# Kernel optimization log

Measured on AMD Instinct MI355X. Metric: run time of the kernel, lower is better.

## Reference

```python
import jax, jax.numpy as jnp
import numpy as np

GAMMA = 0.1
B, C, H, W = 8, 64, 64, 64
CINT = C // 8


def setup_inputs() -> dict:
    key = jax.random.key(0)
    ks = jax.random.split(key, 5)
    x = jax.random.normal(ks[0], (B, C, H, W), dtype=jnp.float32)
    Wq = jax.random.normal(ks[1], (CINT, C), dtype=jnp.float32) * 0.05
    Wk = jax.random.normal(ks[2], (CINT, C), dtype=jnp.float32) * 0.05
    Wv = jax.random.normal(ks[3], (CINT, C), dtype=jnp.float32) * 0.05
    Wout = jax.random.normal(ks[4], (C, CINT), dtype=jnp.float32) * 0.05
    return {"x": x, "Wq": Wq, "Wk": Wk, "Wv": Wv, "Wout": Wout}


def reference(x, Wq, Wk, Wv, Wout):
    b, c, h, w = x.shape
    n = h * w
    cint = Wq.shape[0]
    xf = x.reshape(b, c, n)                               # [B,C,N]
    q = jnp.einsum('ic,bcn->bin', Wq, xf)                 # [B,Cint,N]
    k = jnp.einsum('ic,bcn->bin', Wk, xf)
    v = jnp.einsum('ic,bcn->bin', Wv, xf)
    # scores[b, n, m] = q[b,:,n] . k[b,:,m]; softmax over dim=1 (the n axis)
    scores = jnp.einsum('bin,bim->bnm', q, k) / jnp.sqrt(jnp.asarray(cint, x.dtype))
    att = jax.nn.softmax(scores, axis=1)                  # [B,N,N], softmax over rows
    att_out = jnp.einsum('bin,bnm->bim', v, att)          # [B,Cint,N]
    out = jnp.einsum('ci,bim->bcm', Wout, att_out)        # [B,C,N]
    return x + out.reshape(b, c, h, w) * GAMMA
```

## Files before the change

### kernel.cpp

```cpp
#include <hip/hip_runtime.h>
#include <math.h>

#define BB 8
#define CC 64
#define NN 4096
#define CI 8
#define GAMMA 0.1f
#define SCALE (1.44269504088896f * 0.35355339059327f)
#define NSPLIT 8

typedef float v4f  __attribute__((ext_vector_type(4)));
typedef float v16f __attribute__((ext_vector_type(16)));
typedef __bf16 bf16x8 __attribute__((ext_vector_type(8)));
typedef unsigned int u32x2 __attribute__((ext_vector_type(2)));

__device__ __forceinline__ float fast_exp2(float x) {
    return __builtin_amdgcn_exp2f(x);
}

__device__ __forceinline__ unsigned int cvt_pk_bf16(float lo, float hi) {
    unsigned int r;
    asm("v_cvt_pk_bf16_f32 %0, %1, %2" : "=v"(r) : "v"(lo), "v"(hi));
    return r;
}

__global__ __launch_bounds__(256) void qkv_kernel(
        const float* __restrict__ x,
        const float* __restrict__ Wq, const float* __restrict__ Wk,
        const float* __restrict__ Wv,
        __bf16* __restrict__ qbh, __bf16* __restrict__ kbh,
        __bf16* __restrict__ vbh, float* __restrict__ attab) {
    __shared__ float sw[3 * CI * CC];
    __shared__ float xt[CC * 36];
    __shared__ unsigned short sq[32 * 8];
    __shared__ unsigned short sk[32 * 8];
    const int t = threadIdx.x;
    const int b  = blockIdx.y;
    const int n0 = blockIdx.x * 32;

    for (int idx = t; idx < CI * CC; idx += 256) {
        sw[idx]                = Wq[idx];
        sw[CI * CC + idx]      = Wk[idx] * SCALE;
        sw[2 * CI * CC + idx]  = Wv[idx];
    }
    {
        const float* xb = x + ((size_t)b * CC) * NN + n0;
#pragma unroll
        for (int j = 0; j < 2; ++j) {
            int u = t + j * 256;
            int c = u >> 3, n4 = u & 7;
            v4f xv = *(const v4f*)(xb + (size_t)c * NN + n4 * 4);
            *(v4f*)(xt + c * 36 + n4 * 4) = xv;
        }
    }
    int lin = (blockIdx.y * (NN / 32) + blockIdx.x) * 256 + t;
    for (int idx = lin; idx < BB * 9 * NN; idx += BB * NN * CI) attab[idx] = 0.f;
    __syncthreads();

    const int i  = t >> 5;
    const int nl = t & 31;
    const int n = n0 + nl;
    const v4f* wq4 = (const v4f*)(sw + i * CC);
    const v4f* wk4 = (const v4f*)(sw + CI * CC + i * CC);
    const v4f* wv4 = (const v4f*)(sw + 2 * CI * CC + i * CC);
    float qa = 0.f, ka = 0.f, va = 0.f;
#pragma unroll 4
    for (int c4 = 0; c4 < CC / 4; ++c4) {
        v4f wq = wq4[c4], wk = wk4[c4], wv = wv4[c4];
        float x0 = xt[(c4 * 4 + 0) * 36 + nl];
        float x1 = xt[(c4 * 4 + 1) * 36 + nl];
        float x2 = xt[(c4 * 4 + 2) * 36 + nl];
        float x3 = xt[(c4 * 4 + 3) * 36 + nl];
        qa = fmaf(wq.x, x0, qa); ka = fmaf(wk.x, x0, ka); va = fmaf(wv.x, x0, va);
        qa = fmaf(wq.y, x1, qa); ka = fmaf(wk.y, x1, ka); va = fmaf(wv.y, x1, va);
        qa = fmaf(wq.z, x2, qa); ka = fmaf(wk.z, x2, ka); va = fmaf(wv.z, x2, va);
        qa = fmaf(wq.w, x3, qa); ka = fmaf(wk.w, x3, ka); va = fmaf(wv.w, x3, va);
    }
    __bf16 vb = (__bf16)va;
    vbh[((size_t)b * CI + i) * NN + n] = vb;
    __bf16 qb = (__bf16)qa, kb2 = (__bf16)ka;
    sq[nl * 8 + i] = *(unsigned short*)&qb;
    sk[nl * 8 + i] = *(unsigned short*)&kb2;
    __syncthreads();
    if (t < 32) {
        *(uint4*)(qbh + ((size_t)b * NN + n0 + t) * 8) = *(const uint4*)(sq + t * 8);
        *(uint4*)(kbh + ((size_t)b * NN + n0 + t) * 8) = *(const uint4*)(sk + t * 8);
    }
}

__global__ __launch_bounds__(256) void att_kernel(
        const __bf16* __restrict__ qbh, const __bf16* __restrict__ kbh,
        const __bf16* __restrict__ vbh, float* __restrict__ attab) {
    const int t = threadIdx.x;
    const int w    = t >> 6;
    const int l    = t & 63;
    const int ln   = l & 31;
    const int hi   = l >> 5;
    const int b  = blockIdx.z;
    const int m0 = blockIdx.x * 128 + w * 32;
    const int nbase = blockIdx.y * (NN / NSPLIT);
    const int NCH = (NN / NSPLIT) / 32;

    bf16x8 zero8;
#pragma unroll
    for (int z = 0; z < 8; ++z) zero8[z] = (__bf16)0.0f;
    const v16f vzero = {0.f,0.f,0.f,0.f,0.f,0.f,0.f,0.f,
                        0.f,0.f,0.f,0.f,0.f,0.f,0.f,0.f};

    bf16x8 kfragB = hi ? zero8
                       : *(const bf16x8*)(kbh + ((size_t)b * NN + m0 + ln) * 8);

    const __bf16* qrow = qbh + (size_t)b * NN * 8;
    const __bf16* vrow = vbh + ((size_t)b * CI + (ln & 7)) * NN;

    v16f acc = vzero;
    float den = 0.f;

    for (int ch = 0; ch < NCH; ++ch) {
        const int nc = nbase + ch * 32;
        bf16x8 qf  = *(const bf16x8*)(qrow + (size_t)(nc + ln) * 8);
        bf16x8 va0 = *(const bf16x8*)(vrow + nc + hi * 8);
        bf16x8 va1 = *(const bf16x8*)(vrow + nc + 16 + hi * 8);

        v16f S = __builtin_amdgcn_mfma_f32_32x32x16_bf16(qf, kfragB, vzero,
                                                         0, 0, 0);

        float e0  = fast_exp2(S[0]),  e1  = fast_exp2(S[1]);
        float e2  = fast_exp2(S[2]),  e3  = fast_exp2(S[3]);
        float e4  = fast_exp2(S[4]),  e5  = fast_exp2(S[5]);
        float e6  = fast_exp2(S[6]),  e7  = fast_exp2(S[7]);
        float e8  = fast_exp2(S[8]),  e9  = fast_exp2(S[9]);
        float e10 = fast_exp2(S[10]), e11 = fast_exp2(S[11]);
        float e12 = fast_exp2(S[12]), e13 = fast_exp2(S[13]);
        float e14 = fast_exp2(S[14]), e15 = fast_exp2(S[15]);

        den += (((e0 + e1) + (e2 + e3)) + ((e4 + e5) + (e6 + e7)))
             + (((e8 + e9) + (e10 + e11)) + ((e12 + e13) + (e14 + e15)));

        unsigned int pk0 = cvt_pk_bf16(e0,  e1);
        unsigned int pk1 = cvt_pk_bf16(e2,  e3);
        unsigned int pk2 = cvt_pk_bf16(e4,  e5);
        unsigned int pk3 = cvt_pk_bf16(e6,  e7);
        unsigned int pk4 = cvt_pk_bf16(e8,  e9);
        unsigned int pk5 = cvt_pk_bf16(e10, e11);
        unsigned int pk6 = cvt_pk_bf16(e12, e13);
        unsigned int pk7 = cvt_pk_bf16(e14, e15);

        u32x2 r02 = __builtin_amdgcn_permlane32_swap(pk0, pk2, false, false);
        u32x2 r13 = __builtin_amdgcn_permlane32_swap(pk1, pk3, false, false);
        u32x2 r46 = __builtin_amdgcn_permlane32_swap(pk4, pk6, false, false);
        u32x2 r57 = __builtin_amdgcn_permlane32_swap(pk5, pk7, false, false);

        union { unsigned int u[4]; bf16x8 f; } e0f, e1f;
        e0f.u[0] = r02[0]; e0f.u[1] = r13[0]; e0f.u[2] = r02[1]; e0f.u[3] = r13[1];
        e1f.u[0] = r46[0]; e1f.u[1] = r57[0]; e1f.u[2] = r46[1]; e1f.u[3] = r57[1];

        acc = __builtin_amdgcn_mfma_f32_32x32x16_bf16(va0, e0f.f, acc, 0, 0, 0);
        acc = __builtin_amdgcn_mfma_f32_32x32x16_bf16(va1, e1f.f, acc, 0, 0, 0);
    }

    float* ap = attab + (size_t)b * 9 * NN + m0 + ln;
#pragma unroll
    for (int r = 0; r < 4; ++r)
        atomicAdd(ap + (size_t)(r + 4 * hi) * NN, acc[r]);
    float dtot = den + __shfl_xor(den, 32, 64);
    if (hi == 0)
        atomicAdd(ap + (size_t)8 * NN, dtot);
}

__global__ __launch_bounds__(256) void out_kernel(
        const float* __restrict__ x, const float* __restrict__ Wout,
        const float* __restrict__ attab, float* __restrict__ out) {
    const int t = threadIdx.x;
    const int c = blockIdx.y;
    const int b = blockIdx.z;
    const int m = (blockIdx.x * 256 + t) * 4;
    const float* ap = attab + (size_t)b * 9 * NN + m;
    v4f sum = *(const v4f*)(ap + (size_t)8 * NN);
    v4f s = {0.f, 0.f, 0.f, 0.f};
#pragma unroll
    for (int i = 0; i < CI; ++i) {
        float wgt = Wout[c * CI + i];
        v4f a = *(const v4f*)(ap + (size_t)i * NN);
        s.x = fmaf(wgt, a.x, s.x);
        s.y = fmaf(wgt, a.y, s.y);
        s.z = fmaf(wgt, a.z, s.z);
        s.w = fmaf(wgt, a.w, s.w);
    }
    size_t o = ((size_t)b * CC + c) * NN + m;
    v4f xv = *(const v4f*)(x + o);
    v4f r;
    r.x = xv.x + GAMMA * (s.x / sum.x);
    r.y = xv.y + GAMMA * (s.y / sum.y);
    r.z = xv.z + GAMMA * (s.z / sum.z);
    r.w = xv.w + GAMMA * (s.w / sum.w);
    *(v4f*)(out + o) = r;
}

extern "C" void kernel_launch(void* const* d_in, const int* in_sizes, int n_in,
                              void* d_out, int out_size, void* d_ws, size_t ws_size,
                              hipStream_t stream) {
    const float* x    = (const float*)d_in[0];
    const float* Wq   = (const float*)d_in[1];
    const float* Wk   = (const float*)d_in[2];
    const float* Wv   = (const float*)d_in[3];
    const float* Wout = (const float*)d_in[4];
    float* out = (float*)d_out;

    __bf16* qbh = (__bf16*)d_ws;
    __bf16* kbh = qbh + (size_t)BB * NN * 8;
    __bf16* vbh = kbh + (size_t)BB * NN * 8;
    float* attab = (float*)(vbh + (size_t)BB * NN * 8);

    qkv_kernel<<<dim3(NN / 32, BB), 256, 0, stream>>>(x, Wq, Wk, Wv, qbh, kbh, vbh, attab);
    att_kernel<<<dim3(NN / 128, NSPLIT, BB), 256, 0, stream>>>(qbh, kbh, vbh, attab);
    out_kernel<<<dim3(NN / 1024, CC, BB), 256, 0, stream>>>(x, Wout, attab, out);
}
```

Before: 116.1 us.

## Process four key tiles per wave to reuse Q/V loads and interleave MFMA with exp

Each wave now handles 128 output columns (four 32-column key tiles) instead of 32. The Q and V fragments loaded per chunk are reused across four score MFMAs, and score MFMAs are interleaved with the exp/convert work of the previous tile. This cuts global load traffic per unit of work and hides MFMA latency. The cost is a 4x smaller grid (512 blocks), which lowers parallelism, plus higher register pressure from four accumulators.

```diff
diff --git a/kernel.cpp b/kernel.cpp
--- a/kernel.cpp
+++ b/kernel.cpp
@@ -88,6 +88,37 @@
     }
 }
 
+__device__ __forceinline__ void tile_proc(const v16f S, v16f& acc, float& den,
+                                          bf16x8 va0, bf16x8 va1) {
+    float e0  = fast_exp2(S[0]),  e1  = fast_exp2(S[1]);
+    float e2  = fast_exp2(S[2]),  e3  = fast_exp2(S[3]);
+    float e4  = fast_exp2(S[4]),  e5  = fast_exp2(S[5]);
+    float e6  = fast_exp2(S[6]),  e7  = fast_exp2(S[7]);
+    float e8  = fast_exp2(S[8]),  e9  = fast_exp2(S[9]);
+    float e10 = fast_exp2(S[10]), e11 = fast_exp2(S[11]);
+    float e12 = fast_exp2(S[12]), e13 = fast_exp2(S[13]);
+    float e14 = fast_exp2(S[14]), e15 = fast_exp2(S[15]);
+    den += (((e0 + e1) + (e2 + e3)) + ((e4 + e5) + (e6 + e7)))
+         + (((e8 + e9) + (e10 + e11)) + ((e12 + e13) + (e14 + e15)));
+    unsigned int pk0 = cvt_pk_bf16(e0,  e1);
+    unsigned int pk1 = cvt_pk_bf16(e2,  e3);
+    unsigned int pk2 = cvt_pk_bf16(e4,  e5);
+    unsigned int pk3 = cvt_pk_bf16(e6,  e7);
+    unsigned int pk4 = cvt_pk_bf16(e8,  e9);
+    unsigned int pk5 = cvt_pk_bf16(e10, e11);
+    unsigned int pk6 = cvt_pk_bf16(e12, e13);
+    unsigned int pk7 = cvt_pk_bf16(e14, e15);
+    u32x2 r02 = __builtin_amdgcn_permlane32_swap(pk0, pk2, false, false);
+    u32x2 r13 = __builtin_amdgcn_permlane32_swap(pk1, pk3, false, false);
+    u32x2 r46 = __builtin_amdgcn_permlane32_swap(pk4, pk6, false, false);
+    u32x2 r57 = __builtin_amdgcn_permlane32_swap(pk5, pk7, false, false);
+    union { unsigned int u[4]; bf16x8 f; } e0f, e1f;
+    e0f.u[0] = r02[0]; e0f.u[1] = r13[0]; e0f.u[2] = r02[1]; e0f.u[3] = r13[1];
+    e1f.u[0] = r46[0]; e1f.u[1] = r57[0]; e1f.u[2] = r46[1]; e1f.u[3] = r57[1];
+    acc = __builtin_amdgcn_mfma_f32_32x32x16_bf16(va0, e0f.f, acc, 0, 0, 0);
+    acc = __builtin_amdgcn_mfma_f32_32x32x16_bf16(va1, e1f.f, acc, 0, 0, 0);
+}
+
 __global__ __launch_bounds__(256) void att_kernel(
         const __bf16* __restrict__ qbh, const __bf16* __restrict__ kbh,
         const __bf16* __restrict__ vbh, float* __restrict__ attab) {
@@ -97,7 +128,7 @@
     const int ln   = l & 31;
     const int hi   = l >> 5;
     const int b  = blockIdx.z;
-    const int m0 = blockIdx.x * 128 + w * 32;
+    const int m0 = blockIdx.x * 512 + w * 128;
     const int nbase = blockIdx.y * (NN / NSPLIT);
     const int NCH = (NN / NSPLIT) / 32;
 
@@ -107,14 +138,17 @@
     const v16f vzero = {0.f,0.f,0.f,0.f,0.f,0.f,0.f,0.f,
                         0.f,0.f,0.f,0.f,0.f,0.f,0.f,0.f};
 
-    bf16x8 kfragB = hi ? zero8
-                       : *(const bf16x8*)(kbh + ((size_t)b * NN + m0 + ln) * 8);
+    const __bf16* kb = kbh + ((size_t)b * NN + m0 + ln) * 8;
+    bf16x8 kB0 = hi ? zero8 : *(const bf16x8*)(kb);
+    bf16x8 kB1 = hi ? zero8 : *(const bf16x8*)(kb + 32 * 8);
+    bf16x8 kB2 = hi ? zero8 : *(const bf16x8*)(kb + 64 * 8);
+    bf16x8 kB3 = hi ? zero8 : *(const bf16x8*)(kb + 96 * 8);
 
     const __bf16* qrow = qbh + (size_t)b * NN * 8;
     const __bf16* vrow = vbh + ((size_t)b * CI + (ln & 7)) * NN;
 
-    v16f acc = vzero;
-    float den = 0.f;
+    v16f acc0 = vzero, acc1 = vzero, acc2 = vzero, acc3 = vzero;
+    float den0 = 0.f, den1 = 0.f, den2 = 0.f, den3 = 0.f;
 
     for (int ch = 0; ch < NCH; ++ch) {
         const int nc = nbase + ch * 32;
@@ -122,50 +156,34 @@
         bf16x8 va0 = *(const bf16x8*)(vrow + nc + hi * 8);
         bf16x8 va1 = *(const bf16x8*)(vrow + nc + 16 + hi * 8);
 
-        v16f S = __builtin_amdgcn_mfma_f32_32x32x16_bf16(qf, kfragB, vzero,
-                                                         0, 0, 0);
-
-        float e0  = fast_exp2(S[0]),  e1  = fast_exp2(S[1]);
-        float e2  = fast_exp2(S[2]),  e3  = fast_exp2(S[3]);
-        float e4  = fast_exp2(S[4]),  e5  = fast_exp2(S[5]);
-        float e6  = fast_exp2(S[6]),  e7  = fast_exp2(S[7]);
-        float e8  = fast_exp2(S[8]),  e9  = fast_exp2(S[9]);
-        float e10 = fast_exp2(S[10]), e11 = fast_exp2(S[11]);
-        float e12 = fast_exp2(S[12]), e13 = fast_exp2(S[13]);
-        float e14 = fast_exp2(S[14]), e15 = fast_exp2(S[15]);
-
-        den += (((e0 + e1) + (e2 + e3)) + ((e4 + e5) + (e6 + e7)))
-             + (((e8 + e9) + (e10 + e11)) + ((e12 + e13) + (e14 + e15)));
-
-        unsigned int pk0 = cvt_pk_bf16(e0,  e1);
-        unsigned int pk1 = cvt_pk_bf16(e2,  e3);
-        unsigned int pk2 = cvt_pk_bf16(e4,  e5);
-        unsigned int pk3 = cvt_pk_bf16(e6,  e7);
-        unsigned int pk4 = cvt_pk_bf16(e8,  e9);
-        unsigned int pk5 = cvt_pk_bf16(e10, e11);
-        unsigned int pk6 = cvt_pk_bf16(e12, e13);
-        unsigned int pk7 = cvt_pk_bf16(e14, e15);
-
-        u32x2 r02 = __builtin_amdgcn_permlane32_swap(pk0, pk2, false, false);
-        u32x2 r13 = __builtin_amdgcn_permlane32_swap(pk1, pk3, false, false);
-        u32x2 r46 = __builtin_amdgcn_permlane32_swap(pk4, pk6, false, false);
-        u32x2 r57 = __builtin_amdgcn_permlane32_swap(pk5, pk7, false, false);
-
-        union { unsigned int u[4]; bf16x8 f; } e0f, e1f;
-        e0f.u[0] = r02[0]; e0f.u[1] = r13[0]; e0f.u[2] = r02[1]; e0f.u[3] = r13[1];
-        e1f.u[0] = r46[0]; e1f.u[1] = r57[0]; e1f.u[2] = r46[1]; e1f.u[3] = r57[1];
-
-        acc = __builtin_amdgcn_mfma_f32_32x32x16_bf16(va0, e0f.f, acc, 0, 0, 0);
-        acc = __builtin_amdgcn_mfma_f32_32x32x16_bf16(va1, e1f.f, acc, 0, 0, 0);
+        v16f S0 = __builtin_amdgcn_mfma_f32_32x32x16_bf16(qf, kB0, vzero, 0, 0, 0);
+        v16f S1 = __builtin_amdgcn_mfma_f32_32x32x16_bf16(qf, kB1, vzero, 0, 0, 0);
+        tile_proc(S0, acc0, den0, va0, va1);
+        v16f S2 = __builtin_amdgcn_mfma_f32_32x32x16_bf16(qf, kB2, vzero, 0, 0, 0);
+        tile_proc(S1, acc1, den1, va0, va1);
+        v16f S3 = __builtin_amdgcn_mfma_f32_32x32x16_bf16(qf, kB3, vzero, 0, 0, 0);
+        tile_proc(S2, acc2, den2, va0, va1);
+        tile_proc(S3, acc3, den3, va0, va1);
     }
 
     float* ap = attab + (size_t)b * 9 * NN + m0 + ln;
 #pragma unroll
-    for (int r = 0; r < 4; ++r)
-        atomicAdd(ap + (size_t)(r + 4 * hi) * NN, acc[r]);
-    float dtot = den + __shfl_xor(den, 32, 64);
-    if (hi == 0)
-        atomicAdd(ap + (size_t)8 * NN, dtot);
+    for (int r = 0; r < 4; ++r) {
+        atomicAdd(ap      + (size_t)(r + 4 * hi) * NN, acc0[r]);
+        atomicAdd(ap + 32 + (size_t)(r + 4 * hi) * NN, acc1[r]);
+        atomicAdd(ap + 64 + (size_t)(r + 4 * hi) * NN, acc2[r]);
+        atomicAdd(ap + 96 + (size_t)(r + 4 * hi) * NN, acc3[r]);
+    }
+    float d0 = den0 + __shfl_xor(den0, 32, 64);
+    float d1 = den1 + __shfl_xor(den1, 32, 64);
+    float d2 = den2 + __shfl_xor(den2, 32, 64);
+    float d3 = den3 + __shfl_xor(den3, 32, 64);
+    if (hi == 0) {
+        atomicAdd(ap      + (size_t)8 * NN, d0);
+        atomicAdd(ap + 32 + (size_t)8 * NN, d1);
+        atomicAdd(ap + 64 + (size_t)8 * NN, d2);
+        atomicAdd(ap + 96 + (size_t)8 * NN, d3);
+    }
 }
 
 __global__ __launch_bounds__(256) void out_kernel(
@@ -213,6 +231,6 @@
     float* attab = (float*)(vbh + (size_t)BB * NN * 8);
 
     qkv_kernel<<<dim3(NN / 32, BB), 256, 0, stream>>>(x, Wq, Wk, Wv, qbh, kbh, vbh, attab);
-    att_kernel<<<dim3(NN / 128, NSPLIT, BB), 256, 0, stream>>>(qbh, kbh, vbh, attab);
+    att_kernel<<<dim3(NN / 512, NSPLIT, BB), 256, 0, stream>>>(qbh, kbh, vbh, attab);
     out_kernel<<<dim3(NN / 1024, CC, BB), 256, 0, stream>>>(x, Wout, attab, out);
 }
```

New measurement: 109.9 us. 1.06x faster.
